# Kernel tuning notes

Measured on AMD Instinct MI355X. Metric: run time of the kernel, lower is better.

The kernel has to match this reference:

```python
import jax, jax.numpy as jnp
import numpy as np

N = 262144
IF = 256   # indiv_f_dim
CF = 256   # collab_f_dim
D = IF + CF  # d_model = 512
EMB = 256
NUM_SEASONS = 8192


def setup_inputs() -> dict:
    key = jax.random.key(0)
    ks = jax.random.split(key, 20)
    inp = {
        'indiv_f': jax.random.normal(ks[0], (N, IF), jnp.float32),
        'hierarchy_f': jax.random.normal(ks[1], (N, CF), jnp.float32),
        'strength_f': jax.random.normal(ks[2], (N, CF), jnp.float32),
        'recency_f': jax.random.normal(ks[3], (N, CF), jnp.float32),
        'season_ids': jax.random.randint(ks[4], (N,), 0, NUM_SEASONS, jnp.int32),
    }
    s = 0.02
    # Attention_Biased_Walk: attn_fc1 (no bias)
    inp['w_attn1'] = jax.random.normal(ks[5], (1, 2 * CF), jnp.float32) * s
    # MultiHeadAttention (heads=1): q,k,v,out linears (torch Linear: [out,in] + bias)
    inp['Wq'] = jax.random.normal(ks[6], (D, D), jnp.float32) * s
    inp['bq'] = jnp.zeros((D,), jnp.float32)
    inp['Wk'] = jax.random.normal(ks[7], (D, D), jnp.float32) * s
    inp['bk'] = jnp.zeros((D,), jnp.float32)
    inp['Wv'] = jax.random.normal(ks[8], (D, D), jnp.float32) * s
    inp['bv'] = jnp.zeros((D,), jnp.float32)
    inp['Wo'] = jax.random.normal(ks[9], (D, D), jnp.float32) * s
    inp['bo'] = jnp.zeros((D,), jnp.float32)
    # fc: d_model -> emb_dim
    inp['Wfc'] = jax.random.normal(ks[10], (EMB, D), jnp.float32) * s
    inp['bfc'] = jnp.zeros((EMB,), jnp.float32)
    # output_fc: emb_dim -> 1
    inp['Wout'] = jax.random.normal(ks[11], (1, EMB), jnp.float32) * s
    inp['bout'] = jnp.zeros((1,), jnp.float32)
    return inp


def _forward(indiv_f, hierarchy_f, strength_f, recency_f,
             w_attn1, Wq, bq, Wk, bk, Wv, bv, Wo, bo,
             Wfc, bfc, Wout, bout, season_ids):
    H, S, R = hierarchy_f, strength_f, recency_f
    # Attention_Biased_Walk (is_hierarchy & is_strength & is_recency all True).
    # Dropout is identity in eval. leaky_relu default slope 0.01.
    def e(a, b):
        return jax.nn.leaky_relu(jnp.concatenate([a, b], axis=1) @ w_attn1.T, 0.01)  # [N,1]
    e_all = jnp.stack([e(H, S), e(H, R), e(H, H)], axis=2)          # [N,1,3]
    alpha = jax.nn.softmax(e_all, axis=2)                            # [N,1,3]
    v_cand = jnp.stack([S, R, H], axis=2)                            # [N,CF,3]
    agg_collab_f = jnp.sum(alpha * v_cand, axis=2)                   # [N,CF]

    x = jnp.concatenate([indiv_f, agg_collab_f], axis=1)            # [N,D]

    # MultiHeadAttention with bs=n_members, seq_len=1 per member:
    # scores is [bs,1,1,1], softmax over size-1 axis == 1, so attn = v-projection.
    q = x @ Wq.T + bq
    k = x @ Wk.T + bk
    v = x @ Wv.T + bv
    d_k = D  # heads = 1
    scores = jnp.sum(q * k, axis=-1, keepdims=True) / jnp.sqrt(jnp.float32(d_k))  # [N,1]
    attn_w = jax.nn.softmax(scores[..., None], axis=-1)[..., 0]     # == 1.0, kept for fidelity
    attn_out = (attn_w * v) @ Wo.T + bo                              # [N,D]

    member_emb = jax.nn.relu(attn_out @ Wfc.T + bfc)                 # [N,EMB]

    # Per-season mean-pool (vectorized equivalent of the python loop; all seasons present).
    sums = jax.ops.segment_sum(member_emb, season_ids, num_segments=NUM_SEASONS)
    counts = jax.ops.segment_sum(jnp.ones((member_emb.shape[0],), member_emb.dtype),
                                 season_ids, num_segments=NUM_SEASONS)
    team_emb = sums / jnp.maximum(counts, 1.0)[:, None]              # [NUM_SEASONS,EMB]

    return team_emb @ Wout.T + bout                                  # [NUM_SEASONS,1]


def reference(indiv_f, hierarchy_f, strength_f, recency_f, season_ids,
              w_attn1, Wq, bq, Wk, bk, Wv, bv, Wo, bo, Wfc, bfc, Wout, bout):
    return _forward(indiv_f, hierarchy_f, strength_f, recency_f,
                    w_attn1, Wq, bq, Wk, bk, Wv, bv, Wo, bo,
                    Wfc, bfc, Wout, bout, season_ids)
```

## Files before the change

kernel.cpp:

```cpp
#include <hip/hip_runtime.h>
#include <hip/hip_bf16.h>

typedef __bf16 v8bf __attribute__((ext_vector_type(8)));
typedef __bf16 v4bf __attribute__((ext_vector_type(4)));
typedef float  v4f  __attribute__((ext_vector_type(4)));

#define NMEM 262144
#define CFD  256
#define NSEA 8192



__global__ __launch_bounds__(256)
void gemm_nn(const float* __restrict__ A, const float* __restrict__ B,
             float* __restrict__ C, int M, int Nn, int K) {
  __shared__ float As[16][68];
  __shared__ float Bs[16][68];
  const int tid = threadIdx.x;
  const int tx = tid & 15, ty = tid >> 4;
  const int row0 = blockIdx.y * 64, col0 = blockIdx.x * 64;
  const int lr = tid >> 2, lk = (tid & 3) << 2;
  const int br = tid >> 4, bc = (tid & 15) << 2;
  float acc[4][4] = {};
  for (int kk = 0; kk < K; kk += 16) {
    const float4 a4 = *(const float4*)(A + (size_t)(row0 + lr) * K + kk + lk);
    const float4 b4 = *(const float4*)(B + (size_t)(kk + br) * Nn + col0 + bc);
    __syncthreads();
    As[lk + 0][lr] = a4.x; As[lk + 1][lr] = a4.y;
    As[lk + 2][lr] = a4.z; As[lk + 3][lr] = a4.w;
    *(float4*)&Bs[br][bc] = b4;
    __syncthreads();
#pragma unroll
    for (int t = 0; t < 16; ++t) {
      const float4 av = *(const float4*)&As[t][ty << 2];
      const float4 bv = *(const float4*)&Bs[t][tx << 2];
      acc[0][0] += av.x * bv.x; acc[0][1] += av.x * bv.y;
      acc[0][2] += av.x * bv.z; acc[0][3] += av.x * bv.w;
      acc[1][0] += av.y * bv.x; acc[1][1] += av.y * bv.y;
      acc[1][2] += av.y * bv.z; acc[1][3] += av.y * bv.w;
      acc[2][0] += av.z * bv.x; acc[2][1] += av.z * bv.y;
      acc[2][2] += av.z * bv.z; acc[2][3] += av.z * bv.w;
      acc[3][0] += av.w * bv.x; acc[3][1] += av.w * bv.y;
      acc[3][2] += av.w * bv.z; acc[3][3] += av.w * bv.w;
    }
  }
#pragma unroll
  for (int i = 0; i < 4; ++i) {
    const float4 o = make_float4(acc[i][0], acc[i][1], acc[i][2], acc[i][3]);
    *(float4*)(C + (size_t)(row0 + (ty << 2) + i) * Nn + col0 + (tx << 2)) = o;
  }
}

__global__ void bias_dot(const float* __restrict__ W, const float* __restrict__ x,
                         const float* __restrict__ b, float* __restrict__ o, int K) {
  const int i = blockIdx.x, L = threadIdx.x;
  const float* row = W + (size_t)i * K;
  float s = 0.f;
  for (int k = L; k < K; k += 64) s += row[k] * x[k];
#pragma unroll
  for (int m = 32; m; m >>= 1) s += __shfl_xor(s, m, 64);
  if (L == 0) o[i] = s + b[i];
}

__global__ void pack_b(const float* __restrict__ W3, __bf16* __restrict__ Bp) {
  const int t = blockIdx.x * 256 + threadIdx.x;
  const int L = t & 63, kc = (t >> 6) & 15, nt = t >> 10;
  const int n = nt * 16 + (L & 15);
  const int k = kc * 32 + ((L >> 4) << 3);
  const float* src = W3 + n * 512 + k;
  __bf16* dst = Bp + (size_t)t * 8;
#pragma unroll
  for (int j = 0; j < 8; ++j) dst[j] = (__bf16)src[j];
}


__global__ __launch_bounds__(256, 5)
void fused_main(const float* __restrict__ indiv,
                const float* __restrict__ hier,
                const float* __restrict__ stren,
                const float* __restrict__ rec,
                const int*   __restrict__ sid,
                const float* __restrict__ w1,
                const __bf16* __restrict__ Bp,
                const float* __restrict__ b3,
                const float* __restrict__ wout,
                float* __restrict__ sums,
                float* __restrict__ counts) {
  __shared__ __align__(16) char smem[32768];

  const int tid = threadIdx.x;
  const int w = tid >> 6, L = tid & 63;
  const int mbase = blockIdx.x * 64 + w * 16;
  __bf16* const xw = (__bf16*)(smem + (w << 13));

  const float4 w1a = *(const float4*)(w1 + 4 * L);
  const float4 w1b = *(const float4*)(w1 + 256 + 4 * L);

  const float* hrow = hier  + (size_t)mbase * CFD + 4 * L;
  const float* srow = stren + (size_t)mbase * CFD + 4 * L;
  const float* rrow = rec   + (size_t)mbase * CFD + 4 * L;
  float4 Hc = *(const float4*)hrow;
  float4 Sc = *(const float4*)srow;
  float4 Rc = *(const float4*)rrow;
  for (int i = 0; i < 16; ++i) {
    const int nx = (i < 15) ? (i + 1) : 15;
    float4 Hn = *(const float4*)(hrow + nx * CFD);
    float4 Sn = *(const float4*)(srow + nx * CFD);
    float4 Rn = *(const float4*)(rrow + nx * CFD);

    const float pHa = w1a.x*Hc.x + w1a.y*Hc.y + w1a.z*Hc.z + w1a.w*Hc.w;
    const float pSb = w1b.x*Sc.x + w1b.y*Sc.y + w1b.z*Sc.z + w1b.w*Sc.w;
    const float pRb = w1b.x*Rc.x + w1b.y*Rc.y + w1b.z*Rc.z + w1b.w*Rc.w;
    const float pHb = w1b.x*Hc.x + w1b.y*Hc.y + w1b.z*Hc.z + w1b.w*Hc.w;
    float q1 = pHa + pSb;
    float q2 = pHa + pRb;
    float q3 = pHa + pHb;
#pragma unroll
    for (int m = 32; m; m >>= 1) {
      q1 += __shfl_xor(q1, m, 64);
      q2 += __shfl_xor(q2, m, 64);
      q3 += __shfl_xor(q3, m, 64);
    }
    const float e1 = q1 > 0.f ? q1 : 0.01f * q1;
    const float e2 = q2 > 0.f ? q2 : 0.01f * q2;
    const float e3 = q3 > 0.f ? q3 : 0.01f * q3;
    const float mx = fmaxf(e1, fmaxf(e2, e3));
    float a1 = __expf(e1 - mx), a2 = __expf(e2 - mx), a3 = __expf(e3 - mx);
    const float inv = 1.f / (a1 + a2 + a3);
    a1 *= inv; a2 *= inv; a3 *= inv;

    v4bf g;
    g[0] = (__bf16)(a1 * Sc.x + a2 * Rc.x + a3 * Hc.x);
    g[1] = (__bf16)(a1 * Sc.y + a2 * Rc.y + a3 * Hc.y);
    g[2] = (__bf16)(a1 * Sc.z + a2 * Rc.z + a3 * Hc.z);
    g[3] = (__bf16)(a1 * Sc.w + a2 * Rc.w + a3 * Hc.w);
    {
      const int u  = ((L >> 3) << 6) | (((L >> 1) & 3) << 4) | i;
      const int us = u ^ ((u >> 4) & 7);
      *(v4bf*)(xw + us * 8 + ((L & 1) << 2)) = g;
    }

    Hc = Hn; Sc = Sn; Rc = Rn;
  }

  const int ml = L & 15;
  const int qo = (L >> 4) * 8;
  v8bf af[16];
  {
    const float* ip = indiv + (size_t)(mbase + ml) * CFD;
#pragma unroll
    for (int c = 0; c < 8; ++c) {
      const float4 f0 = *(const float4*)(ip + c * 32 + qo);
      const float4 f1 = *(const float4*)(ip + c * 32 + qo + 4);
      v8bf t;
      t[0] = (__bf16)f0.x; t[1] = (__bf16)f0.y; t[2] = (__bf16)f0.z; t[3] = (__bf16)f0.w;
      t[4] = (__bf16)f1.x; t[5] = (__bf16)f1.y; t[6] = (__bf16)f1.z; t[7] = (__bf16)f1.w;
      af[c] = t;
    }
#pragma unroll
    for (int c = 0; c < 8; ++c) {
      const int u  = (c << 6) | L;
      const int us = u ^ ((u >> 4) & 7);
      af[8 + c] = *(const v8bf*)(xw + us * 8);
    }
  }

  float p0 = 0.f, p1 = 0.f, p2 = 0.f, p3 = 0.f;
  const uint4* bsrc = (const uint4*)Bp;
  uint4* bl = (uint4*)smem;
  const v8bf* btile = (const v8bf*)smem;
  for (int nt = 0; nt < 16; ++nt) {
    __syncthreads();
#pragma unroll
    for (int j = 0; j < 4; ++j)
      bl[tid + j * 256] = bsrc[nt * 1024 + tid + j * 256];
    __syncthreads();

    v4f acc = {0.f, 0.f, 0.f, 0.f};
#pragma unroll
    for (int c = 0; c < 16; ++c) {
      const v8bf bf = btile[c * 64 + L];
      acc = __builtin_amdgcn_mfma_f32_16x16x32_bf16(af[c], bf, acc, 0, 0, 0);
    }
    const float b3n = b3[nt * 16 + ml];
    const float wn  = wout[nt * 16 + ml];
    p0 += fmaxf(acc[0] + b3n, 0.f) * wn;
    p1 += fmaxf(acc[1] + b3n, 0.f) * wn;
    p2 += fmaxf(acc[2] + b3n, 0.f) * wn;
    p3 += fmaxf(acc[3] + b3n, 0.f) * wn;
  }

#pragma unroll
  for (int m = 8; m; m >>= 1) {
    p0 += __shfl_xor(p0, m, 64);
    p1 += __shfl_xor(p1, m, 64);
    p2 += __shfl_xor(p2, m, 64);
    p3 += __shfl_xor(p3, m, 64);
  }
  const int r = ml;
  if (r < 4) {
    const float pv = (r == 0) ? p0 : (r == 1) ? p1 : (r == 2) ? p2 : p3;
    const int mem = mbase + (L >> 4) * 4 + r;
    const int s = sid[mem];
    atomicAdd(&sums[s], pv);
    atomicAdd(&counts[s], 1.0f);
  }
}

__global__ void finalize_k(const float* __restrict__ sums,
                           const float* __restrict__ counts,
                           const float* __restrict__ bout,
                           float* __restrict__ out) {
  const int s = blockIdx.x * 256 + threadIdx.x;
  if (s < NSEA) out[s] = sums[s] / fmaxf(counts[s], 1.0f) + bout[0];
}


extern "C" void kernel_launch(void* const* d_in, const int* in_sizes, int n_in,
                              void* d_out, int out_size, void* d_ws, size_t ws_size,
                              hipStream_t stream) {
  (void)in_sizes; (void)n_in; (void)out_size; (void)ws_size;
  const float* indiv = (const float*)d_in[0];
  const float* hier  = (const float*)d_in[1];
  const float* stren = (const float*)d_in[2];
  const float* rec   = (const float*)d_in[3];
  const int*   sid   = (const int*)d_in[4];
  const float* w1    = (const float*)d_in[5];
  const float* Wv    = (const float*)d_in[10];
  const float* bv    = (const float*)d_in[11];
  const float* Wo    = (const float*)d_in[12];
  const float* bo    = (const float*)d_in[13];
  const float* Wfc   = (const float*)d_in[14];
  const float* bfc   = (const float*)d_in[15];
  const float* wout  = (const float*)d_in[16];
  const float* bout  = (const float*)d_in[17];
  float* out = (float*)d_out;

  char* ws = (char*)d_ws;
  float*  T1   = (float*)(ws + 0);
  float*  W3   = (float*)(ws + 1048576);
  float*  bc   = (float*)(ws + 1572864);
  float*  b3   = (float*)(ws + 1574912);
  __bf16* Bp   = (__bf16*)(ws + 1575936);
  float*  sums = (float*)(ws + 1838080);
  float*  cnts = (float*)(ws + 1870848);

  hipMemsetAsync(ws + 1838080, 0, 65536, stream);

  gemm_nn<<<dim3(8, 8), 256, 0, stream>>>(Wo,  Wv, T1, 512, 512, 512);
  bias_dot<<<512, 64, 0, stream>>>(Wo, bv, bo, bc, 512);
  gemm_nn<<<dim3(8, 4), 256, 0, stream>>>(Wfc, T1, W3, 256, 512, 512);
  bias_dot<<<256, 64, 0, stream>>>(Wfc, bc, bfc, b3, 512);
  pack_b<<<64, 256, 0, stream>>>(W3, Bp);

  fused_main<<<NMEM / 64, 256, 0, stream>>>(indiv, hier, stren, rec, sid, w1,
                                            Bp, b3, wout, sums, cnts);
  finalize_k<<<NSEA / 256, 256, 0, stream>>>(sums, cnts, bout, out);
}
```

Before: 1.016 ms.

## Restructure attention-walk gather per lane, prefetch B tiles, split MFMA accumulators

The attention-walk stage now gives each group of four lanes one member row, doing the dot products with local accumulation and a two-step shuffle instead of a full 64-lane reduction for every row. It then reloads the row to write 8-wide bf16 vectors into shared memory. The B-tile loop prefetches the next tile into registers while the current one is consumed. Two independent MFMA accumulator chains replace the single dependent chain. Occupancy drops from 5 to 3 blocks per SIMD to make room for the extra registers, and the H/S/R rows are now read twice, with the second read likely served from cache.

After: 1.321 ms. +30.1%, slower.

```diff
diff --git a/kernel.cpp b/kernel.cpp
--- a/kernel.cpp
+++ b/kernel.cpp
@@ -74,7 +74,7 @@
 }
 
 
-__global__ __launch_bounds__(256, 5)
+__global__ __launch_bounds__(256, 3)
 void fused_main(const float* __restrict__ indiv,
                 const float* __restrict__ hier,
                 const float* __restrict__ stren,
@@ -93,54 +93,71 @@
   const int mbase = blockIdx.x * 64 + w * 16;
   __bf16* const xw = (__bf16*)(smem + (w << 13));
 
-  const float4 w1a = *(const float4*)(w1 + 4 * L);
-  const float4 w1b = *(const float4*)(w1 + 256 + 4 * L);
-
-  const float* hrow = hier  + (size_t)mbase * CFD + 4 * L;
-  const float* srow = stren + (size_t)mbase * CFD + 4 * L;
-  const float* rrow = rec   + (size_t)mbase * CFD + 4 * L;
-  float4 Hc = *(const float4*)hrow;
-  float4 Sc = *(const float4*)srow;
-  float4 Rc = *(const float4*)rrow;
-  for (int i = 0; i < 16; ++i) {
-    const int nx = (i < 15) ? (i + 1) : 15;
-    float4 Hn = *(const float4*)(hrow + nx * CFD);
-    float4 Sn = *(const float4*)(srow + nx * CFD);
-    float4 Rn = *(const float4*)(rrow + nx * CFD);
-
-    const float pHa = w1a.x*Hc.x + w1a.y*Hc.y + w1a.z*Hc.z + w1a.w*Hc.w;
-    const float pSb = w1b.x*Sc.x + w1b.y*Sc.y + w1b.z*Sc.z + w1b.w*Sc.w;
-    const float pRb = w1b.x*Rc.x + w1b.y*Rc.y + w1b.z*Rc.z + w1b.w*Rc.w;
-    const float pHb = w1b.x*Hc.x + w1b.y*Hc.y + w1b.z*Hc.z + w1b.w*Hc.w;
-    float q1 = pHa + pSb;
-    float q2 = pHa + pRb;
-    float q3 = pHa + pHb;
-#pragma unroll
-    for (int m = 32; m; m >>= 1) {
-      q1 += __shfl_xor(q1, m, 64);
-      q2 += __shfl_xor(q2, m, 64);
-      q3 += __shfl_xor(q3, m, 64);
-    }
-    const float e1 = q1 > 0.f ? q1 : 0.01f * q1;
-    const float e2 = q2 > 0.f ? q2 : 0.01f * q2;
-    const float e3 = q3 > 0.f ? q3 : 0.01f * q3;
-    const float mx = fmaxf(e1, fmaxf(e2, e3));
-    float a1 = __expf(e1 - mx), a2 = __expf(e2 - mx), a3 = __expf(e3 - mx);
-    const float inv = 1.f / (a1 + a2 + a3);
-    a1 *= inv; a2 *= inv; a3 *= inv;
-
-    v4bf g;
-    g[0] = (__bf16)(a1 * Sc.x + a2 * Rc.x + a3 * Hc.x);
-    g[1] = (__bf16)(a1 * Sc.y + a2 * Rc.y + a3 * Hc.y);
-    g[2] = (__bf16)(a1 * Sc.z + a2 * Rc.z + a3 * Hc.z);
-    g[3] = (__bf16)(a1 * Sc.w + a2 * Rc.w + a3 * Hc.w);
-    {
-      const int u  = ((L >> 3) << 6) | (((L >> 1) & 3) << 4) | i;
-      const int us = u ^ ((u >> 4) & 7);
-      *(v4bf*)(xw + us * 8 + ((L & 1) << 2)) = g;
-    }
-
-    Hc = Hn; Sc = Sn; Rc = Rn;
+  const int i4  = L >> 2;
+  const int sub = L & 3;
+  const float* hrow = hier  + (size_t)(mbase + i4) * CFD + sub * 64;
+  const float* srow = stren + (size_t)(mbase + i4) * CFD + sub * 64;
+  const float* rrow = rec   + (size_t)(mbase + i4) * CFD + sub * 64;
+  const float* wa = w1 + sub * 64;
+  const float* wb = w1 + 256 + sub * 64;
+
+  float4 aHa = {0.f,0.f,0.f,0.f}, aSb = {0.f,0.f,0.f,0.f};
+  float4 aRb = {0.f,0.f,0.f,0.f}, aHb = {0.f,0.f,0.f,0.f};
+#pragma unroll 4
+  for (int t = 0; t < 16; ++t) {
+    const float4 h = *(const float4*)(hrow + 4 * t);
+    const float4 s = *(const float4*)(srow + 4 * t);
+    const float4 r = *(const float4*)(rrow + 4 * t);
+    const float4 a = *(const float4*)(wa + 4 * t);
+    const float4 b = *(const float4*)(wb + 4 * t);
+    aHa.x += a.x*h.x; aHa.y += a.y*h.y; aHa.z += a.z*h.z; aHa.w += a.w*h.w;
+    aSb.x += b.x*s.x; aSb.y += b.y*s.y; aSb.z += b.z*s.z; aSb.w += b.w*s.w;
+    aRb.x += b.x*r.x; aRb.y += b.y*r.y; aRb.z += b.z*r.z; aRb.w += b.w*r.w;
+    aHb.x += b.x*h.x; aHb.y += b.y*h.y; aHb.z += b.z*h.z; aHb.w += b.w*h.w;
+  }
+  float pHa = (aHa.x + aHa.y) + (aHa.z + aHa.w);
+  float pSb = (aSb.x + aSb.y) + (aSb.z + aSb.w);
+  float pRb = (aRb.x + aRb.y) + (aRb.z + aRb.w);
+  float pHb = (aHb.x + aHb.y) + (aHb.z + aHb.w);
+#pragma unroll
+  for (int m = 1; m <= 2; m <<= 1) {
+    pHa += __shfl_xor(pHa, m, 64);
+    pSb += __shfl_xor(pSb, m, 64);
+    pRb += __shfl_xor(pRb, m, 64);
+    pHb += __shfl_xor(pHb, m, 64);
+  }
+  const float q1 = pHa + pSb;
+  const float q2 = pHa + pRb;
+  const float q3 = pHa + pHb;
+  const float e1 = q1 > 0.f ? q1 : 0.01f * q1;
+  const float e2 = q2 > 0.f ? q2 : 0.01f * q2;
+  const float e3 = q3 > 0.f ? q3 : 0.01f * q3;
+  const float mx = fmaxf(e1, fmaxf(e2, e3));
+  float a1 = __expf(e1 - mx), a2 = __expf(e2 - mx), a3 = __expf(e3 - mx);
+  const float inv = 1.f / (a1 + a2 + a3);
+  a1 *= inv; a2 *= inv; a3 *= inv;
+
+#pragma unroll
+  for (int j = 0; j < 8; ++j) {
+    const float4 s0 = *(const float4*)(srow + 8 * j);
+    const float4 s1 = *(const float4*)(srow + 8 * j + 4);
+    const float4 r0 = *(const float4*)(rrow + 8 * j);
+    const float4 r1 = *(const float4*)(rrow + 8 * j + 4);
+    const float4 h0 = *(const float4*)(hrow + 8 * j);
+    const float4 h1 = *(const float4*)(hrow + 8 * j + 4);
+    v8bf g;
+    g[0] = (__bf16)(a1 * s0.x + a2 * r0.x + a3 * h0.x);
+    g[1] = (__bf16)(a1 * s0.y + a2 * r0.y + a3 * h0.y);
+    g[2] = (__bf16)(a1 * s0.z + a2 * r0.z + a3 * h0.z);
+    g[3] = (__bf16)(a1 * s0.w + a2 * r0.w + a3 * h0.w);
+    g[4] = (__bf16)(a1 * s1.x + a2 * r1.x + a3 * h1.x);
+    g[5] = (__bf16)(a1 * s1.y + a2 * r1.y + a3 * h1.y);
+    g[6] = (__bf16)(a1 * s1.z + a2 * r1.z + a3 * h1.z);
+    g[7] = (__bf16)(a1 * s1.w + a2 * r1.w + a3 * h1.w);
+    const int c = sub * 2 + (j >> 2);
+    const int u = (c << 6) | ((j & 3) << 4) | i4;
+    const int us = u ^ ((u >> 4) & 7);
+    *(v8bf*)(xw + us * 8) = g;
   }
 
   const int ml = L & 15;
@@ -149,19 +166,19 @@
   {
     const float* ip = indiv + (size_t)(mbase + ml) * CFD;
 #pragma unroll
-    for (int c = 0; c < 8; ++c) {
-      const float4 f0 = *(const float4*)(ip + c * 32 + qo);
-      const float4 f1 = *(const float4*)(ip + c * 32 + qo + 4);
+    for (int cc = 0; cc < 8; ++cc) {
+      const float4 f0 = *(const float4*)(ip + cc * 32 + qo);
+      const float4 f1 = *(const float4*)(ip + cc * 32 + qo + 4);
       v8bf t;
       t[0] = (__bf16)f0.x; t[1] = (__bf16)f0.y; t[2] = (__bf16)f0.z; t[3] = (__bf16)f0.w;
       t[4] = (__bf16)f1.x; t[5] = (__bf16)f1.y; t[6] = (__bf16)f1.z; t[7] = (__bf16)f1.w;
-      af[c] = t;
-    }
-#pragma unroll
-    for (int c = 0; c < 8; ++c) {
-      const int u  = (c << 6) | L;
+      af[cc] = t;
+    }
+#pragma unroll
+    for (int cc = 0; cc < 8; ++cc) {
+      const int u  = (cc << 6) | L;
       const int us = u ^ ((u >> 4) & 7);
-      af[8 + c] = *(const v8bf*)(xw + us * 8);
+      af[8 + cc] = *(const v8bf*)(xw + us * 8);
     }
   }
 
@@ -169,25 +186,35 @@
   const uint4* bsrc = (const uint4*)Bp;
   uint4* bl = (uint4*)smem;
   const v8bf* btile = (const v8bf*)smem;
+  uint4 breg0 = bsrc[tid];
+  uint4 breg1 = bsrc[tid + 256];
+  uint4 breg2 = bsrc[tid + 512];
+  uint4 breg3 = bsrc[tid + 768];
   for (int nt = 0; nt < 16; ++nt) {
     __syncthreads();
-#pragma unroll
-    for (int j = 0; j < 4; ++j)
-      bl[tid + j * 256] = bsrc[nt * 1024 + tid + j * 256];
-    __syncthreads();
-
-    v4f acc = {0.f, 0.f, 0.f, 0.f};
-#pragma unroll
-    for (int c = 0; c < 16; ++c) {
-      const v8bf bf = btile[c * 64 + L];
-      acc = __builtin_amdgcn_mfma_f32_16x16x32_bf16(af[c], bf, acc, 0, 0, 0);
+    bl[tid      ] = breg0;
+    bl[tid + 256] = breg1;
+    bl[tid + 512] = breg2;
+    bl[tid + 768] = breg3;
+    if (nt < 15) {
+      const uint4* nb = bsrc + (nt + 1) * 1024 + tid;
+      breg0 = nb[0]; breg1 = nb[256]; breg2 = nb[512]; breg3 = nb[768];
+    }
+    __syncthreads();
+
+    v4f acc0 = {0.f, 0.f, 0.f, 0.f};
+    v4f acc1 = {0.f, 0.f, 0.f, 0.f};
+#pragma unroll
+    for (int c = 0; c < 16; c += 2) {
+      acc0 = __builtin_amdgcn_mfma_f32_16x16x32_bf16(af[c],     btile[c * 64 + L],       acc0, 0, 0, 0);
+      acc1 = __builtin_amdgcn_mfma_f32_16x16x32_bf16(af[c + 1], btile[(c + 1) * 64 + L], acc1, 0, 0, 0);
     }
     const float b3n = b3[nt * 16 + ml];
     const float wn  = wout[nt * 16 + ml];
-    p0 += fmaxf(acc[0] + b3n, 0.f) * wn;
-    p1 += fmaxf(acc[1] + b3n, 0.f) * wn;
-    p2 += fmaxf(acc[2] + b3n, 0.f) * wn;
-    p3 += fmaxf(acc[3] + b3n, 0.f) * wn;
+    p0 += fmaxf(acc0[0] + acc1[0] + b3n, 0.f) * wn;
+    p1 += fmaxf(acc0[1] + acc1[1] + b3n, 0.f) * wn;
+    p2 += fmaxf(acc0[2] + acc1[2] + b3n, 0.f) * wn;
+    p3 += fmaxf(acc0[3] + acc1[3] + b3n, 0.f) * wn;
   }
 
 #pragma unroll
```
